# Performance work log

Measured on AMD Instinct MI355X. Metric: run time of the kernel, lower is better.

Reference implementation:

```python
import jax, jax.numpy as jnp
import numpy as np

TREE_DEPTH = 6
IN_F, OUT_F = 1024, 1024
BATCH = 2048
N_LEAVES = 2 ** TREE_DEPTH
N_NODES = N_LEAVES - 1


def _tree_routes(depth):
    """Static routing table: for each leaf, the decision-node index visited at
    each depth and whether the leaf takes the sigmoid (1) or 1-sigmoid (0) branch.
    Mirrors the torch traversal: node = 2*node + 1 + bit; bits of leaf id LSB-first."""
    n_leaves = 2 ** depth
    idx = np.zeros((n_leaves, depth), dtype=np.int32)
    pos = np.zeros((n_leaves, depth), dtype=bool)
    for l in range(n_leaves):
        node, index = 0, l
        for d in range(depth):
            idx[l, d] = node
            pos[l, d] = (index % 2 == 0)
            node = node * 2 + 1 + index % 2
            index >>= 1
    return idx, pos

ROUTE_IDX, ROUTE_POS = _tree_routes(TREE_DEPTH)


def setup_inputs() -> dict:
    key = jax.random.key(0)
    kx, kwd, kwl = jax.random.split(key, 3)
    scale = 0.02  # keep sigmoid/softmax logits in a sane range
    x = jax.random.normal(kx, (BATCH, IN_F), dtype=jnp.float32)
    Wd = jax.random.normal(kwd, (N_NODES, IN_F), dtype=jnp.float32) * scale
    bd = jnp.zeros((N_NODES,), dtype=jnp.float32)
    Wl = jax.random.normal(kwl, (N_LEAVES, OUT_F, IN_F), dtype=jnp.float32) * scale
    bl = jnp.zeros((N_LEAVES, OUT_F), dtype=jnp.float32)
    return {"x": x, "Wd": Wd, "bd": bd, "Wl": Wl, "bl": bl}


def reference(x, Wd, bd, Wl, bl):
    # All decision node probabilities in one GEMM: [B, n_nodes]
    dprob = jax.nn.sigmoid(x @ Wd.T + bd)
    # Gather per-leaf path probs [B, L, depth] and take path product -> routing [B, L]
    path = dprob[:, ROUTE_IDX]                      # [B, L, D]
    path = jnp.where(ROUTE_POS, path, 1.0 - path)
    routing = jnp.prod(path, axis=-1)               # [B, L]
    # All leaf experts in one batched GEMM: [B, L, out], softmax over out (torch dim=1)
    leaf_logits = jnp.einsum('bi,loi->blo', x, Wl) + bl
    leaves = jax.nn.softmax(leaf_logits, axis=-1)
    # Routing-weighted sum over leaves
    return jnp.einsum('bl,blo->bo', routing, leaves)
```

## Files before the change

### kernel.cpp

```cpp
#include <hip/hip_runtime.h>
#include <hip/hip_bf16.h>

#define BATCH 2048
#define KD 1024
#define ND 1024
#define NLEAF 64
#define BM 256
#define BN 256
#define BKT 32
#define NKT (KD / BKT)

typedef __attribute__((ext_vector_type(8))) short bf16x8;
typedef __attribute__((ext_vector_type(4))) float f32x4;
typedef __attribute__((ext_vector_type(4))) _Float16 f16x4;

#define WLB_OFF 0ULL
#define XB_OFF  134217728ULL
#define RT_OFF  138412032ULL
#define LG_OFF  138936320ULL

__device__ __forceinline__ unsigned short f2bf(float f) {
  unsigned int u = __float_as_uint(f);
  u += 0x7fffu + ((u >> 16) & 1u);
  return (unsigned short)(u >> 16);
}

__device__ __forceinline__ void gload_lds16(const void* g, void* l) {
  __builtin_amdgcn_global_load_lds(
      (const __attribute__((address_space(1))) unsigned int*)g,
      (__attribute__((address_space(3))) unsigned int*)l, 16, 0, 0);
}

__global__ void __launch_bounds__(256) convert_kernel(
    const float* __restrict__ Wl, const float* __restrict__ x,
    unsigned short* __restrict__ wlb, unsigned short* __restrict__ xb) {
  const long long WL4 = 16777216LL;
  const long long X4  = 524288LL;
  long long i = (long long)blockIdx.x * 256 + threadIdx.x;
  const long long stride = (long long)gridDim.x * 256;
  for (; i < WL4 + X4; i += stride) {
    float4 v;
    if (i < WL4) v = ((const float4*)Wl)[i];
    else         v = ((const float4*)x)[i - WL4];
    ushort4 o;
    o.x = f2bf(v.x); o.y = f2bf(v.y); o.z = f2bf(v.z); o.w = f2bf(v.w);
    if (i < WL4) ((ushort4*)wlb)[i] = o;
    else         ((ushort4*)xb)[i - WL4] = o;
  }
}

__global__ void __launch_bounds__(256) routing_kernel(
    const float* __restrict__ x, const float* __restrict__ Wd,
    const float* __restrict__ bd, float* __restrict__ rt) {
  __shared__ float xs[4][KD];
  __shared__ float sdp[4][64];
  const int tid = threadIdx.x;
  const int b0 = blockIdx.x * 4;
  const float4* xsrc = (const float4*)(x + (size_t)b0 * KD);
  float4* xdst = (float4*)&xs[0][0];
  for (int i = tid; i < KD; i += 256) xdst[i] = xsrc[i];
  __syncthreads();
  const int wv = tid >> 6, ln = tid & 63;
  const int b = b0 + wv;
  if (ln < 63) {
    const float4* wrow = (const float4*)(Wd + (size_t)ln * KD);
    const float4* xr = (const float4*)&xs[wv][0];
    float4 a = {0.f, 0.f, 0.f, 0.f};
    for (int k = 0; k < KD / 4; ++k) {
      float4 w = wrow[k], xv = xr[k];
      a.x += w.x * xv.x; a.y += w.y * xv.y; a.z += w.z * xv.z; a.w += w.w * xv.w;
    }
    float z = a.x + a.y + a.z + a.w + bd[ln];
    sdp[wv][ln] = 1.f / (1.f + __expf(-z));
  }
  __syncthreads();
  float prod = 1.f;
  int node = 0, index = ln;
  for (int d = 0; d < 6; ++d) {
    float pv = sdp[wv][node];
    prod *= (index & 1) ? (1.f - pv) : pv;
    node = node * 2 + 1 + (index & 1);
    index >>= 1;
  }
  rt[(size_t)b * NLEAF + ln] = prod;
}

__global__ void __launch_bounds__(512, 2) gemm_kernel(
    const unsigned short* __restrict__ A, const unsigned short* __restrict__ B,
    _Float16* __restrict__ C, int ntile) {
  extern __shared__ char smem[];
  const int tid = threadIdx.x;
  const int w = tid >> 6, ln = tid & 63;
  const int wm = w >> 2, wn = w & 3;
  const int g = ln >> 4, r16 = ln & 15;
  const int bid = blockIdx.x;
  const int j = bid >> 3;
  const int bm = (j & 7) * BM;
  const int bn = (((j >> 3) << 3) + (bid & 7)) * BN;
  const long long ldc = (long long)ntile * 256;

  const int rS = tid >> 2;
  const int cS = tid & 3;
  const int csrc = cS ^ ((rS >> 1) & 3);
  const unsigned short* ga0 = A + (size_t)(bm + rS) * KD + csrc * 8;
  const unsigned short* ga1 = ga0 + (size_t)128 * KD;
  const unsigned short* gb0 = B + (size_t)(bn + rS) * KD + csrc * 8;
  const unsigned short* gb1 = gb0 + (size_t)128 * KD;
  const int ldsw = w * 1024;

  auto STAGE = [&](int tile) {
    char* base = smem + (tile & 3) * 32768;
    const size_t ko = (size_t)tile * BKT;
    gload_lds16(ga0 + ko, base + ldsw);
    gload_lds16(ga1 + ko, base + 8192 + ldsw);
    gload_lds16(gb0 + ko, base + 16384 + ldsw);
    gload_lds16(gb1 + ko, base + 24576 + ldsw);
  };

  int offA[8], offB[4];
#pragma unroll
  for (int mi = 0; mi < 8; ++mi) {
    const int row = wm * 128 + mi * 16 + r16;
    offA[mi] = row * 64 + (g ^ ((row >> 1) & 3)) * 16;
  }
#pragma unroll
  for (int ni = 0; ni < 4; ++ni) {
    const int row = wn * 64 + ni * 16 + r16;
    offB[ni] = 16384 + row * 64 + (g ^ ((row >> 1) & 3)) * 16;
  }

  f32x4 acc[8][4];
#pragma unroll
  for (int mi = 0; mi < 8; ++mi)
#pragma unroll
    for (int ni = 0; ni < 4; ++ni) acc[mi][ni] = (f32x4){0.f, 0.f, 0.f, 0.f};

  STAGE(0); STAGE(1); STAGE(2);
  asm volatile("s_waitcnt vmcnt(8)" ::: "memory");
  asm volatile("s_barrier" ::: "memory");

  for (int t = 0; t < NKT; ++t) {
    if (t + 3 < NKT) STAGE(t + 3);
    const char* buf = smem + (t & 3) * 32768;
    bf16x8 af[8], bfr[4];
#pragma unroll
    for (int mi = 0; mi < 8; ++mi) af[mi] = *(const bf16x8*)(buf + offA[mi]);
#pragma unroll
    for (int ni = 0; ni < 4; ++ni) bfr[ni] = *(const bf16x8*)(buf + offB[ni]);
    __builtin_amdgcn_s_setprio(1);
#pragma unroll
    for (int mi = 0; mi < 8; ++mi)
#pragma unroll
      for (int ni = 0; ni < 4; ++ni)
        acc[mi][ni] = __builtin_amdgcn_mfma_f32_16x16x32_bf16(
            af[mi], bfr[ni], acc[mi][ni], 0, 0, 0);
    __builtin_amdgcn_s_setprio(0);
    __builtin_amdgcn_sched_barrier(0);
    if (t + 3 < NKT) {
      asm volatile("s_waitcnt vmcnt(8)" ::: "memory");
    } else if (t + 2 < NKT) {
      asm volatile("s_waitcnt vmcnt(4)" ::: "memory");
    } else if (t + 1 < NKT) {
      asm volatile("s_waitcnt vmcnt(0)" ::: "memory");
    }
    if (t + 1 < NKT) asm volatile("s_barrier" ::: "memory");
  }

#pragma unroll
  for (int mi = 0; mi < 8; ++mi)
#pragma unroll
    for (int q = 0; q < 4; ++q) {
      const long long grow = bm + wm * 128 + mi * 16 + g * 4 + q;
#pragma unroll
      for (int ni = 0; ni < 4; ++ni) {
        const int gcol = bn + wn * 64 + ni * 16 + r16;
        C[grow * ldc + gcol] = (_Float16)acc[mi][ni][q];
      }
    }
}

__global__ void __launch_bounds__(256) smax_kernel(
    const _Float16* __restrict__ Cg, const float* __restrict__ rt,
    const float* __restrict__ bl, float* __restrict__ out,
    int lpg, int l0, int first) {
  __shared__ float redm[4], reds[4];
  __shared__ float rts[64];
  const int tid = threadIdx.x;
  const int b = blockIdx.x;
  const int w = tid >> 6, ln = tid & 63;
  const int c0 = tid * 4;
  if (tid < lpg) rts[tid] = rt[(size_t)b * NLEAF + l0 + tid];
  __syncthreads();
  float oacc[4] = {0.f, 0.f, 0.f, 0.f};
  const long long ldc = (long long)lpg * ND;

  for (int jj = 0; jj < lpg; ++jj) {
    const int l = l0 + jj;
    const f16x4 h = *(const f16x4*)(Cg + (size_t)b * ldc + jj * ND + c0);
    const float4 blv = *(const float4*)(bl + (size_t)l * ND + c0);
    float v[4];
    v[0] = (float)h[0] + blv.x; v[1] = (float)h[1] + blv.y;
    v[2] = (float)h[2] + blv.z; v[3] = (float)h[3] + blv.w;
    float m = fmaxf(fmaxf(v[0], v[1]), fmaxf(v[2], v[3]));
#pragma unroll
    for (int off = 1; off < 64; off <<= 1) m = fmaxf(m, __shfl_xor(m, off));
    if (ln == 0) redm[w] = m;
    __syncthreads();
    m = fmaxf(fmaxf(redm[0], redm[1]), fmaxf(redm[2], redm[3]));
    float e[4], s = 0.f;
#pragma unroll
    for (int k = 0; k < 4; ++k) { e[k] = __expf(v[k] - m); s += e[k]; }
#pragma unroll
    for (int off = 1; off < 64; off <<= 1) s += __shfl_xor(s, off);
    if (ln == 0) reds[w] = s;
    __syncthreads();
    const float S = reds[0] + reds[1] + reds[2] + reds[3];
    const float coef = rts[jj] / S;
#pragma unroll
    for (int k = 0; k < 4; ++k) oacc[k] += coef * e[k];
  }

  float* orow = out + (size_t)b * ND + c0;
  if (first) {
    *(float4*)orow = (float4){oacc[0], oacc[1], oacc[2], oacc[3]};
  } else {
    float4 p = *(const float4*)orow;
    p.x += oacc[0]; p.y += oacc[1]; p.z += oacc[2]; p.w += oacc[3];
    *(float4*)orow = p;
  }
}

extern "C" void kernel_launch(void* const* d_in, const int* in_sizes, int n_in,
                              void* d_out, int out_size, void* d_ws, size_t ws_size,
                              hipStream_t stream) {
  const float* x  = (const float*)d_in[0];
  const float* Wd = (const float*)d_in[1];
  const float* bd = (const float*)d_in[2];
  const float* Wl = (const float*)d_in[3];
  const float* bl = (const float*)d_in[4];
  float* out = (float*)d_out;
  char* ws = (char*)d_ws;
  unsigned short* wlb = (unsigned short*)(ws + WLB_OFF);
  unsigned short* xb  = (unsigned short*)(ws + XB_OFF);
  float* rt           = (float*)(ws + RT_OFF);
  _Float16* lg        = (_Float16*)(ws + LG_OFF);

  convert_kernel<<<2048, 256, 0, stream>>>(Wl, x, wlb, xb);
  routing_kernel<<<BATCH / 4, 256, 0, stream>>>(x, Wd, bd, rt);
  hipFuncSetAttribute((const void*)gemm_kernel,
                      hipFuncAttributeMaxDynamicSharedMemorySize, 131072);

  const int ngrp = (ws_size >= LG_OFF + (size_t)BATCH * NLEAF * ND * 2) ? 1 : 4;
  const int lpg = NLEAF / ngrp;
  const int ntile = lpg * (ND / BN) * 4 / 4;
  for (int grp = 0; grp < ngrp; ++grp) {
    gemm_kernel<<<8 * ntile, 512, 131072, stream>>>(
        xb, wlb + (size_t)grp * lpg * ND * KD, lg, ntile);
    smax_kernel<<<BATCH, 256, 0, stream>>>(lg, rt, bl, out,
                                           lpg, grp * lpg, grp == 0);
  }
}
```

Measured before the change: 521.2 us.

## Split GEMM k-step into two MFMA halves and drop softmax max pass

The GEMM main loop is split into two halves. Each half loads half of the A fragments and issues half of the next tile's global-to-LDS loads, so loads are interleaved with MFMA work and fewer A fragment registers are live at once. The softmax kernel drops the max-subtraction pass and processes two leaves per iteration with double-buffered reduction slots, halving the barriers. Skipping the max subtraction is only safe because the logits are small, so it risks overflow for larger inputs.

```diff
diff --git a/kernel.cpp b/kernel.cpp
--- a/kernel.cpp
+++ b/kernel.cpp
@@ -108,11 +108,15 @@
   const unsigned short* gb1 = gb0 + (size_t)128 * KD;
   const int ldsw = w * 1024;
 
-  auto STAGE = [&](int tile) {
+  auto STAGE_A = [&](int tile) {
     char* base = smem + (tile & 3) * 32768;
     const size_t ko = (size_t)tile * BKT;
     gload_lds16(ga0 + ko, base + ldsw);
     gload_lds16(ga1 + ko, base + 8192 + ldsw);
+  };
+  auto STAGE_B = [&](int tile) {
+    char* base = smem + (tile & 3) * 32768;
+    const size_t ko = (size_t)tile * BKT;
     gload_lds16(gb0 + ko, base + 16384 + ldsw);
     gload_lds16(gb1 + ko, base + 24576 + ldsw);
   };
@@ -135,25 +139,45 @@
 #pragma unroll
     for (int ni = 0; ni < 4; ++ni) acc[mi][ni] = (f32x4){0.f, 0.f, 0.f, 0.f};
 
-  STAGE(0); STAGE(1); STAGE(2);
+  STAGE_A(0); STAGE_B(0);
+  STAGE_A(1); STAGE_B(1);
+  STAGE_A(2); STAGE_B(2);
   asm volatile("s_waitcnt vmcnt(8)" ::: "memory");
   asm volatile("s_barrier" ::: "memory");
 
   for (int t = 0; t < NKT; ++t) {
-    if (t + 3 < NKT) STAGE(t + 3);
     const char* buf = smem + (t & 3) * 32768;
-    bf16x8 af[8], bfr[4];
-#pragma unroll
-    for (int mi = 0; mi < 8; ++mi) af[mi] = *(const bf16x8*)(buf + offA[mi]);
+    bf16x8 af[4], bfr[4];
 #pragma unroll
     for (int ni = 0; ni < 4; ++ni) bfr[ni] = *(const bf16x8*)(buf + offB[ni]);
+#pragma unroll
+    for (int mi = 0; mi < 4; ++mi) af[mi] = *(const bf16x8*)(buf + offA[mi]);
+    if (t + 3 < NKT) STAGE_A(t + 3);
+    asm volatile("s_barrier" ::: "memory");
+    asm volatile("s_waitcnt lgkmcnt(0)" ::: "memory");
+    __builtin_amdgcn_sched_barrier(0);
     __builtin_amdgcn_s_setprio(1);
 #pragma unroll
-    for (int mi = 0; mi < 8; ++mi)
+    for (int mi = 0; mi < 4; ++mi)
 #pragma unroll
       for (int ni = 0; ni < 4; ++ni)
         acc[mi][ni] = __builtin_amdgcn_mfma_f32_16x16x32_bf16(
             af[mi], bfr[ni], acc[mi][ni], 0, 0, 0);
+    __builtin_amdgcn_s_setprio(0);
+    __builtin_amdgcn_sched_barrier(0);
+#pragma unroll
+    for (int mi = 0; mi < 4; ++mi) af[mi] = *(const bf16x8*)(buf + offA[mi + 4]);
+    if (t + 3 < NKT) STAGE_B(t + 3);
+    asm volatile("s_barrier" ::: "memory");
+    asm volatile("s_waitcnt lgkmcnt(0)" ::: "memory");
+    __builtin_amdgcn_sched_barrier(0);
+    __builtin_amdgcn_s_setprio(1);
+#pragma unroll
+    for (int mi = 0; mi < 4; ++mi)
+#pragma unroll
+      for (int ni = 0; ni < 4; ++ni)
+        acc[mi + 4][ni] = __builtin_amdgcn_mfma_f32_16x16x32_bf16(
+            af[mi], bfr[ni], acc[mi + 4][ni], 0, 0, 0);
     __builtin_amdgcn_s_setprio(0);
     __builtin_amdgcn_sched_barrier(0);
     if (t + 3 < NKT) {
@@ -183,7 +207,7 @@
     const _Float16* __restrict__ Cg, const float* __restrict__ rt,
     const float* __restrict__ bl, float* __restrict__ out,
     int lpg, int l0, int first) {
-  __shared__ float redm[4], reds[4];
+  __shared__ float reds[2][2][4];
   __shared__ float rts[64];
   const int tid = threadIdx.x;
   const int b = blockIdx.x;
@@ -194,30 +218,32 @@
   float oacc[4] = {0.f, 0.f, 0.f, 0.f};
   const long long ldc = (long long)lpg * ND;
 
-  for (int jj = 0; jj < lpg; ++jj) {
-    const int l = l0 + jj;
-    const f16x4 h = *(const f16x4*)(Cg + (size_t)b * ldc + jj * ND + c0);
-    const float4 blv = *(const float4*)(bl + (size_t)l * ND + c0);
-    float v[4];
-    v[0] = (float)h[0] + blv.x; v[1] = (float)h[1] + blv.y;
-    v[2] = (float)h[2] + blv.z; v[3] = (float)h[3] + blv.w;
-    float m = fmaxf(fmaxf(v[0], v[1]), fmaxf(v[2], v[3]));
-#pragma unroll
-    for (int off = 1; off < 64; off <<= 1) m = fmaxf(m, __shfl_xor(m, off));
-    if (ln == 0) redm[w] = m;
+  for (int jj = 0; jj < lpg; jj += 2) {
+    const int par = (jj >> 1) & 1;
+    const f16x4 h0 = *(const f16x4*)(Cg + (size_t)b * ldc + jj * ND + c0);
+    const f16x4 h1 = *(const f16x4*)(Cg + (size_t)b * ldc + (jj + 1) * ND + c0);
+    const float4 bv0 = *(const float4*)(bl + (size_t)(l0 + jj) * ND + c0);
+    const float4 bv1 = *(const float4*)(bl + (size_t)(l0 + jj + 1) * ND + c0);
+    float e0[4], e1[4], s0 = 0.f, s1 = 0.f;
+    e0[0] = __expf((float)h0[0] + bv0.x); e0[1] = __expf((float)h0[1] + bv0.y);
+    e0[2] = __expf((float)h0[2] + bv0.z); e0[3] = __expf((float)h0[3] + bv0.w);
+    e1[0] = __expf((float)h1[0] + bv1.x); e1[1] = __expf((float)h1[1] + bv1.y);
+    e1[2] = __expf((float)h1[2] + bv1.z); e1[3] = __expf((float)h1[3] + bv1.w);
+#pragma unroll
+    for (int k = 0; k < 4; ++k) { s0 += e0[k]; s1 += e1[k]; }
+#pragma unroll
+    for (int off = 1; off < 64; off <<= 1) {
+      s0 += __shfl_xor(s0, off);
+      s1 += __shfl_xor(s1, off);
+    }
+    if (ln == 0) { reds[par][0][w] = s0; reds[par][1][w] = s1; }
     __syncthreads();
-    m = fmaxf(fmaxf(redm[0], redm[1]), fmaxf(redm[2], redm[3]));
-    float e[4], s = 0.f;
-#pragma unroll
-    for (int k = 0; k < 4; ++k) { e[k] = __expf(v[k] - m); s += e[k]; }
-#pragma unroll
-    for (int off = 1; off < 64; off <<= 1) s += __shfl_xor(s, off);
-    if (ln == 0) reds[w] = s;
-    __syncthreads();
-    const float S = reds[0] + reds[1] + reds[2] + reds[3];
-    const float coef = rts[jj] / S;
-#pragma unroll
-    for (int k = 0; k < 4; ++k) oacc[k] += coef * e[k];
+    const float S0 = reds[par][0][0] + reds[par][0][1] + reds[par][0][2] + reds[par][0][3];
+    const float S1 = reds[par][1][0] + reds[par][1][1] + reds[par][1][2] + reds[par][1][3];
+    const float c0f = rts[jj] / S0;
+    const float c1f = rts[jj + 1] / S1;
+#pragma unroll
+    for (int k = 0; k < 4; ++k) oacc[k] += c0f * e0[k] + c1f * e1[k];
   }
 
   float* orow = out + (size_t)b * ND + c0;
@@ -252,7 +278,7 @@
 
   const int ngrp = (ws_size >= LG_OFF + (size_t)BATCH * NLEAF * ND * 2) ? 1 : 4;
   const int lpg = NLEAF / ngrp;
-  const int ntile = lpg * (ND / BN) * 4 / 4;
+  const int ntile = lpg * (ND / BN);
   for (int grp = 0; grp < ngrp; ++grp) {
     gemm_kernel<<<8 * ntile, 512, 131072, stream>>>(
         xb, wlb + (size_t)grp * lpg * ND * KD, lg, ntile);
```

New measurement: 507.3 us. 2.7% less time.
